# Kernel tuning notes

Measured on AMD Instinct MI355X. Metric: run time of the kernel, lower is better.

The kernel has to match this reference:

```python
import jax, jax.numpy as jnp
import numpy as np

N = 40000   # num nodes
C = 128     # in_channels
H = 8       # num_heads
D = C // H  # head_dim = 16
E = 640000  # num edges
FF = 4 * C


def layer_norm(x, g, b, eps=1e-5):
    m = jnp.mean(x, axis=-1, keepdims=True)
    v = jnp.mean((x - m) ** 2, axis=-1, keepdims=True)
    return (x - m) / jnp.sqrt(v + eps) * g + b


def setup_inputs() -> dict:
    key = jax.random.key(0)
    ks = jax.random.split(key, 16)
    s = 0.02
    x = jax.random.normal(ks[0], (N, C), dtype=jnp.float32)
    edge_index = jax.random.randint(ks[1], (2, E), 0, N, dtype=jnp.int64)
    return {
        'x': x,
        'edge_index': edge_index,
        'Wq': jax.random.normal(ks[2], (C, C), jnp.float32) * s,
        'bq': jnp.zeros((C,), jnp.float32),
        'Wk': jax.random.normal(ks[3], (C, C), jnp.float32) * s,
        'bk': jnp.zeros((C,), jnp.float32),
        'Wv': jax.random.normal(ks[4], (C, C), jnp.float32) * s,
        'bv': jnp.zeros((C,), jnp.float32),
        'Wo': jax.random.normal(ks[5], (C, C), jnp.float32) * s,
        'bo': jnp.zeros((C,), jnp.float32),
        'ln1_g': jnp.ones((C,), jnp.float32),
        'ln1_b': jnp.zeros((C,), jnp.float32),
        'ln2_g': jnp.ones((C,), jnp.float32),
        'ln2_b': jnp.zeros((C,), jnp.float32),
        'W1': jax.random.normal(ks[6], (C, FF), jnp.float32) * s,
        'b1': jnp.zeros((FF,), jnp.float32),
        'W2': jax.random.normal(ks[7], (FF, C), jnp.float32) * s,
        'b2': jnp.zeros((C,), jnp.float32),
    }


def reference(x, edge_index, Wq, bq, Wk, bk, Wv, bv, Wo, bo,
              ln1_g, ln1_b, ln2_g, ln2_b, W1, b1, W2, b2):
    residual = x
    xn = layer_norm(x, ln1_g, ln1_b)
    q = (xn @ Wq + bq).reshape(N, H, D)
    k = (xn @ Wk + bk).reshape(N, H, D)
    v = (xn @ Wv + bv).reshape(N, H, D)
    src, dst = edge_index[0], edge_index[1]
    # per-edge scores: [E, H]
    scores = jnp.einsum('ehd,ehd->eh', q[dst], k[src]) / jnp.sqrt(jnp.float32(D))
    # NOTE: faithful to the source — softmax over ALL edges (dim=0), not per-destination
    attn = jax.nn.softmax(scores, axis=0)[:, :, None]          # [E, H, 1]
    weighted = v[src] * attn                                   # [E, H, D]
    aggregated = jax.ops.segment_sum(weighted, dst, num_segments=N)  # [N, H, D]
    out = aggregated.reshape(N, C) @ Wo + bo
    x1 = residual + out
    residual2 = x1
    xn2 = layer_norm(x1, ln2_g, ln2_b)
    ffn = jax.nn.relu(xn2 @ W1 + b1) @ W2 + b2
    return residual2 + ffn
```

## Files before the change

### kernel.cpp

```cpp
#include <hip/hip_runtime.h>
#include <math.h>

#define NNODES 40000
#define CCH    128
#define NH     8
#define HD     16
#define NEDGE  640000
#define NBLK   157
#define FBLK   10000
#define RBLK   40

typedef __attribute__((ext_vector_type(8))) short bf16x8;
typedef __attribute__((ext_vector_type(4))) float f32x4;
typedef __attribute__((ext_vector_type(2))) float f32x2;

__device__ inline unsigned short f2bf(float f) {
  union { float f; unsigned u; } c; c.f = f;
  unsigned r = c.u + 0x7fffu + ((c.u >> 16) & 1u);
  return (unsigned short)(r >> 16);
}
__device__ inline float bflo(unsigned u) { union { unsigned i; float f; } c; c.i = u << 16; return c.f; }
__device__ inline float bfhi(unsigned u) { union { unsigned i; float f; } c; c.i = u & 0xffff0000u; return c.f; }

__device__ inline unsigned char f2fp8(float v) {
#if __has_builtin(__builtin_amdgcn_cvt_pk_fp8_f32)
  return (unsigned char)(__builtin_amdgcn_cvt_pk_fp8_f32(v, v, 0, false) & 0xff);
#else
  union { float f; unsigned u; } c; c.f = v;
  unsigned s = (c.u >> 24) & 0x80;
  int e = (int)((c.u >> 23) & 0xff) - 127;
  unsigned m = c.u & 0x7fffff;
  if (e > 8) return s | 0x7e;
  if (e >= -6) {
    unsigned q = (m + 0x80000) >> 20; unsigned ee = e + 7;
    if (q == 8) { q = 0; ee++; }
    if (ee > 15) return s | 0x7e;
    return s | (ee << 3) | q;
  }
  if (e < -10) return (unsigned char)s;
  float a = fabsf(v); unsigned q = (unsigned)(a * 512.f + 0.5f); if (q > 7) q = 7;
  return s | q;
#endif
}
__device__ inline void fp8x4d(unsigned w, float* o) {
#if __has_builtin(__builtin_amdgcn_cvt_pk_f32_fp8)
  f32x2 lo = __builtin_amdgcn_cvt_pk_f32_fp8((int)w, false);
  f32x2 hi = __builtin_amdgcn_cvt_pk_f32_fp8((int)w, true);
  o[0] = lo[0]; o[1] = lo[1]; o[2] = hi[0]; o[3] = hi[1];
#else
  #pragma unroll
  for (int i = 0; i < 4; i++) {
    unsigned b = (w >> (8 * i)) & 0xff;
    unsigned s = b >> 7, e = (b >> 3) & 15, m = b & 7;
    float v;
    if (e) { union { unsigned u; float f; } c; c.u = ((e + 120) << 23) | (m << 20); v = c.f; }
    else v = m * (1.f / 512.f);
    o[i] = s ? -v : v;
  }
#endif
}

__global__ __launch_bounds__(256) void k_ln_bf(const float* __restrict__ x,
                                               const float* __restrict__ g,
                                               const float* __restrict__ b,
                                               unsigned* __restrict__ out) {
  int wave = threadIdx.x >> 6;
  int lane = threadIdx.x & 63;
  int row  = blockIdx.x * 4 + wave;
  if (row >= NNODES) return;
  const float2* xr = (const float2*)(x + (size_t)row * CCH);
  float2 v = xr[lane];
  float s  = v.x + v.y;
  float ss = v.x * v.x + v.y * v.y;
  #pragma unroll
  for (int d = 1; d < 64; d <<= 1) {
    s  += __shfl_xor(s, d);
    ss += __shfl_xor(ss, d);
  }
  float mean = s * (1.0f / CCH);
  float var  = ss * (1.0f / CCH) - mean * mean;
  float rstd = rsqrtf(var + 1e-5f);
  float2 gg = ((const float2*)g)[lane];
  float2 bb = ((const float2*)b)[lane];
  float ox = (v.x - mean) * rstd * gg.x + bb.x;
  float oy = (v.y - mean) * rstd * gg.y + bb.y;
  out[(size_t)row * 64 + lane] = ((unsigned)f2bf(oy) << 16) | f2bf(ox);
}

__global__ __launch_bounds__(256) void k_wprep(const float* __restrict__ W,
                                               unsigned short* __restrict__ Wt,
                                               int K, int Nc) {
  int idx = blockIdx.x * 256 + threadIdx.x;
  if (idx >= K * Nc) return;
  int n = idx / K, k = idx - n * K;
  Wt[idx] = f2bf(W[(size_t)k * Nc + n]);
}

__global__ __launch_bounds__(256) void k_wprep_wo(const float* __restrict__ W,
                                                  const float* __restrict__ inv,
                                                  unsigned short* __restrict__ Wt) {
  int idx = blockIdx.x * 256 + threadIdx.x;
  if (idx >= CCH * CCH) return;
  int n = idx >> 7, k = idx & 127;
  Wt[idx] = f2bf(W[(size_t)k * CCH + n] * inv[k >> 4]);
}

__global__ __launch_bounds__(256) void k_bcat(const float* __restrict__ bq,
                                              const float* __restrict__ bk,
                                              const float* __restrict__ bv,
                                              float* __restrict__ bqkv) {
  int t = threadIdx.x + blockIdx.x * 256;
  if (t < 128)      bqkv[t] = bq[t];
  else if (t < 256) bqkv[t] = bk[t - 128];
  else if (t < 384) bqkv[t] = bv[t - 256];
}

template <bool RELU, bool RES, int MODE>
__global__ __launch_bounds__(256) void k_mgemm(const unsigned short* __restrict__ A,
                                               const unsigned short* __restrict__ Bt,
                                               const float* __restrict__ bias,
                                               const float* __restrict__ res,
                                               void* __restrict__ outp,
                                               int K, int Nc) {
  __shared__ unsigned short As[64 * 64];
  __shared__ unsigned short Bs[128 * 64];
  const int tid  = threadIdx.x;
  const int row0 = blockIdx.x * 64;
  const int c0   = blockIdx.y * 128;
  const int l    = tid & 63;
  const int w    = tid >> 6;
  const int wr   = w >> 1;
  const int wc   = w & 1;

  f32x4 acc[2][4] = {};

  for (int kc = 0; kc < K; kc += 64) {
    __syncthreads();
    #pragma unroll
    for (int it = 0; it < 2; it++) {
      int idx = it * 256 + tid;
      int r = idx >> 3, s = idx & 7;
      uint4 vv = *(const uint4*)(A + (size_t)(row0 + r) * K + kc + s * 8);
      *(uint4*)(As + r * 64 + ((s ^ (r & 7)) * 8)) = vv;
    }
    #pragma unroll
    for (int it = 0; it < 4; it++) {
      int idx = it * 256 + tid;
      int n = idx >> 3, s = idx & 7;
      uint4 vv = *(const uint4*)(Bt + (size_t)(c0 + n) * K + kc + s * 8);
      *(uint4*)(Bs + n * 64 + ((s ^ (n & 7)) * 8)) = vv;
    }
    __syncthreads();
    #pragma unroll
    for (int kk = 0; kk < 2; kk++) {
      int sb = kk * 4 + (l >> 4);
      bf16x8 af[2], bfr[4];
      #pragma unroll
      for (int mi = 0; mi < 2; mi++) {
        int r = wr * 32 + mi * 16 + (l & 15);
        af[mi] = *(const bf16x8*)(As + r * 64 + ((sb ^ (r & 7)) * 8));
      }
      #pragma unroll
      for (int ni = 0; ni < 4; ni++) {
        int n = wc * 64 + ni * 16 + (l & 15);
        bfr[ni] = *(const bf16x8*)(Bs + n * 64 + ((sb ^ (n & 7)) * 8));
      }
      #pragma unroll
      for (int mi = 0; mi < 2; mi++)
        #pragma unroll
        for (int ni = 0; ni < 4; ni++)
          acc[mi][ni] = __builtin_amdgcn_mfma_f32_16x16x32_bf16(af[mi], bfr[ni], acc[mi][ni], 0, 0, 0);
    }
  }

  #pragma unroll
  for (int mi = 0; mi < 2; mi++) {
    #pragma unroll
    for (int p = 0; p < 4; p++) {
      int r = row0 + wr * 32 + mi * 16 + (l >> 4) * 4 + p;
      #pragma unroll
      for (int ni = 0; ni < 4; ni++) {
        int c = c0 + wc * 64 + ni * 16 + (l & 15);
        float val = acc[mi][ni][p] + bias[c];
        if (RES)  val += res[(size_t)r * Nc + c];
        if (RELU) val = fmaxf(val, 0.f);
        if (MODE == 0)      ((float*)outp)[(size_t)r * Nc + c] = val;
        else if (MODE == 1) ((unsigned short*)outp)[(size_t)r * Nc + c] = f2bf(val);
        else {
          char* rowb = (char*)outp + (size_t)r * 512;
          if (c < 128) *(unsigned short*)(rowb + c * 2) = f2bf(val);
          else         *(unsigned char*)(rowb + 256 + (c - 128)) = f2fp8(val);
        }
      }
    }
  }
}

__global__ __launch_bounds__(256) void k_histrank(const int* __restrict__ ei,
                                                  int* __restrict__ deg,
                                                  int* __restrict__ rank) {
  int e = blockIdx.x * 256 + threadIdx.x;
  if (e >= NEDGE) return;
  rank[e] = atomicAdd(&deg[ei[NEDGE + e]], 1);
}

__global__ __launch_bounds__(256) void k_scan3a(const int* __restrict__ deg,
                                                int* __restrict__ bsum) {
  int i = blockIdx.x * 256 + threadIdx.x;
  int d = (i < NNODES) ? deg[i] : 0;
  #pragma unroll
  for (int s = 1; s < 64; s <<= 1) d += __shfl_xor(d, s);
  __shared__ int ws4[4];
  if ((threadIdx.x & 63) == 0) ws4[threadIdx.x >> 6] = d;
  __syncthreads();
  if (threadIdx.x == 0) bsum[blockIdx.x] = ws4[0] + ws4[1] + ws4[2] + ws4[3];
}

__global__ __launch_bounds__(256) void k_scan3b(const int* __restrict__ bsum,
                                                int* __restrict__ bpre) {
  int t = threadIdx.x;
  int d = (t < NBLK) ? bsum[t] : 0;
  int lane = t & 63, wv = t >> 6;
  int incl = d;
  #pragma unroll
  for (int s = 1; s < 64; s <<= 1) { int o = __shfl_up(incl, s); if (lane >= s) incl += o; }
  __shared__ int wsum[4];
  if (lane == 63) wsum[wv] = incl;
  __syncthreads();
  int base = 0;
  for (int w2 = 0; w2 < wv; w2++) base += wsum[w2];
  if (t < NBLK) bpre[t] = base + incl - d;
}

__global__ __launch_bounds__(256) void k_scan3c(const int* __restrict__ deg,
                                                const int* __restrict__ bpre,
                                                int* __restrict__ off) {
  int t = threadIdx.x;
  int i = blockIdx.x * 256 + t;
  int d = (i < NNODES) ? deg[i] : 0;
  int lane = t & 63, wv = t >> 6;
  int incl = d;
  #pragma unroll
  for (int s = 1; s < 64; s <<= 1) { int o = __shfl_up(incl, s); if (lane >= s) incl += o; }
  __shared__ int wsum[4];
  if (lane == 63) wsum[wv] = incl;
  __syncthreads();
  int base = bpre[blockIdx.x];
  for (int w2 = 0; w2 < wv; w2++) base += wsum[w2];
  int ex = base + incl - d;
  if (i < NNODES) off[i] = ex;
  if (i == 0) off[NNODES] = NEDGE;
}

__global__ __launch_bounds__(256) void k_scatter(const int* __restrict__ ei,
                                                 const int* __restrict__ off,
                                                 const int* __restrict__ rank,
                                                 int* __restrict__ srcs) {
  int e = blockIdx.x * 256 + threadIdx.x;
  if (e >= NEDGE) return;
  srcs[off[ei[NEDGE + e]] + rank[e]] = ei[e];
}

__global__ __launch_bounds__(256) void k_fused(const unsigned char* __restrict__ qkv,
                                               const int* __restrict__ off,
                                               const int* __restrict__ srcs,
                                               unsigned* __restrict__ U,
                                               float* __restrict__ hpart) {
  const int wave = threadIdx.x >> 6;
  const int lane = threadIdx.x & 63;
  const int n  = blockIdx.x * 4 + wave;
  const int g  = lane >> 3;
  const int c8 = lane & 7;

  const uint4* qp = (const uint4*)(qkv + (size_t)n * 512 + c8 * 32);
  uint4 qa = qp[0], qb = qp[1];
  float qf[16];
  qf[0]=bflo(qa.x);  qf[1]=bfhi(qa.x);  qf[2]=bflo(qa.y);  qf[3]=bfhi(qa.y);
  qf[4]=bflo(qa.z);  qf[5]=bfhi(qa.z);  qf[6]=bflo(qa.w);  qf[7]=bfhi(qa.w);
  qf[8]=bflo(qb.x);  qf[9]=bfhi(qb.x);  qf[10]=bflo(qb.y); qf[11]=bfhi(qb.y);
  qf[12]=bflo(qb.z); qf[13]=bfhi(qb.z); qf[14]=bflo(qb.w); qf[15]=bfhi(qb.w);

  float acc[16];
  #pragma unroll
  for (int i = 0; i < 16; i++) acc[i] = 0.f;
  float lsum = 0.f;

  const int i0 = off[n], i1 = off[n + 1];
  for (int jb = i0; jb < i1; jb += 8) {
    int j = jb + g;
    bool valid = j < i1;
    int src = srcs[valid ? j : jb];
    const uint4* kp = (const uint4*)(qkv + (size_t)src * 512 + 256 + c8 * 16);
    uint4 kw = kp[0];
    uint4 vw = kp[8];
    float kf[16], vf[16];
    fp8x4d(kw.x, kf + 0); fp8x4d(kw.y, kf + 4); fp8x4d(kw.z, kf + 8); fp8x4d(kw.w, kf + 12);
    fp8x4d(vw.x, vf + 0); fp8x4d(vw.y, vf + 4); fp8x4d(vw.z, vf + 8); fp8x4d(vw.w, vf + 12);
    float p = 0.f;
    #pragma unroll
    for (int i = 0; i < 16; i++) p += qf[i] * kf[i];
    float w = valid ? __expf(p * 0.25f) : 0.f;
    lsum += w;
    #pragma unroll
    for (int i = 0; i < 16; i++) acc[i] += w * vf[i];
  }

  #pragma unroll
  for (int d = 8; d < 64; d <<= 1) {
    #pragma unroll
    for (int i = 0; i < 16; i++) acc[i] += __shfl_xor(acc[i], d);
    lsum += __shfl_xor(lsum, d);
  }

  __shared__ float wsum[4][8];
  if (lane < 8) {
    wsum[wave][c8] = lsum;
    unsigned o[8];
    #pragma unroll
    for (int i = 0; i < 8; i++)
      o[i] = ((unsigned)f2bf(acc[2 * i + 1]) << 16) | f2bf(acc[2 * i]);
    uint4* up = (uint4*)(U + (size_t)n * 64 + c8 * 8);
    up[0] = make_uint4(o[0], o[1], o[2], o[3]);
    up[1] = make_uint4(o[4], o[5], o[6], o[7]);
  }
  __syncthreads();
  if (threadIdx.x < 8) {
    hpart[blockIdx.x * 8 + threadIdx.x] =
        wsum[0][threadIdx.x] + wsum[1][threadIdx.x] + wsum[2][threadIdx.x] + wsum[3][threadIdx.x];
  }
}

__global__ __launch_bounds__(256) void k_reduce_part(const float* __restrict__ hpart,
                                                     float* __restrict__ dpart) {
  const int t = threadIdx.x;
  const int h = t & 7;
  const int r0 = blockIdx.x * (FBLK / RBLK);
  float s = 0.f;
  for (int r = r0 + (t >> 3); r < r0 + FBLK / RBLK; r += 32) s += hpart[r * 8 + h];
  #pragma unroll
  for (int d = 8; d < 64; d <<= 1) s += __shfl_xor(s, d);
  __shared__ float ws4[4][8];
  int lane = t & 63, wv = t >> 6;
  if (lane < 8) ws4[wv][lane] = s;
  __syncthreads();
  if (t < 8) dpart[blockIdx.x * 8 + t] = ws4[0][t] + ws4[1][t] + ws4[2][t] + ws4[3][t];
}

__global__ __launch_bounds__(64) void k_inv(const float* __restrict__ dpart,
                                            float* __restrict__ inv) {
  int t = threadIdx.x;
  int h = t & 7;
  float s = 0.f;
  for (int r = t >> 3; r < RBLK; r += 8) s += dpart[r * 8 + h];
  #pragma unroll
  for (int d = 8; d < 64; d <<= 1) s += __shfl_xor(s, d);
  if (t < 8) inv[h] = 1.0f / s;
}

extern "C" void kernel_launch(void* const* d_in, const int* in_sizes, int n_in,
                              void* d_out, int out_size, void* d_ws, size_t ws_size,
                              hipStream_t stream) {
  const float* x    = (const float*)d_in[0];
  const int*   ei   = (const int*)d_in[1];
  const float* Wq   = (const float*)d_in[2];
  const float* bq   = (const float*)d_in[3];
  const float* Wk   = (const float*)d_in[4];
  const float* bk   = (const float*)d_in[5];
  const float* Wv   = (const float*)d_in[6];
  const float* bv   = (const float*)d_in[7];
  const float* Wo   = (const float*)d_in[8];
  const float* bo   = (const float*)d_in[9];
  const float* ln1g = (const float*)d_in[10];
  const float* ln1b = (const float*)d_in[11];
  const float* ln2g = (const float*)d_in[12];
  const float* ln2b = (const float*)d_in[13];
  const float* W1   = (const float*)d_in[14];
  const float* b1   = (const float*)d_in[15];
  const float* W2   = (const float*)d_in[16];
  const float* b2   = (const float*)d_in[17];
  float* out = (float*)d_out;

  char* p = (char*)d_ws;
  unsigned short* xn   = (unsigned short*)p; p += (size_t)NNODES * CCH * 2;
  unsigned char*  qkvb = (unsigned char*)p;  p += (size_t)NNODES * 512;
  unsigned short* agg  = (unsigned short*)p; p += (size_t)NNODES * CCH * 2;
  float*          x1   = (float*)p;          p += (size_t)NNODES * CCH * 4;
  unsigned short* ffn1 = (unsigned short*)p; p += (size_t)NNODES * 4 * CCH * 2;
  int* deg    = (int*)p;                     p += (size_t)NNODES * 4 + 256;
  int* off    = (int*)p;                     p += (size_t)(NNODES + 1) * 4 + 256;
  int* rank   = (int*)p;                     p += (size_t)NEDGE * 4;
  int* srcs   = (int*)p;                     p += (size_t)NEDGE * 4;
  int* bsum   = (int*)p;                     p += 256 * 4;
  int* bpre   = (int*)p;                     p += 256 * 4;
  float* hpart = (float*)p;                  p += (size_t)FBLK * 8 * 4;
  float* dpart = (float*)p;                  p += (size_t)RBLK * 8 * 4 + 256;
  float* inv   = (float*)p;                  p += 256;
  float* bqkv  = (float*)p;                  p += 384 * 4 + 256;
  unsigned short* Wqkvt = (unsigned short*)p; p += (size_t)384 * CCH * 2;
  unsigned short* Wot   = (unsigned short*)p; p += (size_t)CCH * CCH * 2;
  unsigned short* W1t   = (unsigned short*)p; p += (size_t)CCH * 4 * CCH * 2;
  unsigned short* W2t   = (unsigned short*)p; p += (size_t)CCH * 4 * CCH * 2;
  unsigned short* xn2 = xn;

  dim3 blk(256);
  dim3 gLN(NNODES / 4);
  dim3 gM(NNODES / 64, 1);
  dim3 gM3(NNODES / 64, 3);
  dim3 gM4(NNODES / 64, 4);
  dim3 gE((NEDGE + 255) / 256);
  dim3 gW64((CCH * CCH + 255) / 256);
  dim3 gW256((CCH * 4 * CCH + 255) / 256);

  hipMemsetAsync(deg, 0, (size_t)NNODES * 4, stream);
  k_histrank<<<gE, blk, 0, stream>>>(ei, deg, rank);
  k_scan3a<<<NBLK, blk, 0, stream>>>(deg, bsum);
  k_scan3b<<<1, blk, 0, stream>>>(bsum, bpre);
  k_scan3c<<<NBLK, blk, 0, stream>>>(deg, bpre, off);
  k_scatter<<<gE, blk, 0, stream>>>(ei, off, rank, srcs);

  k_wprep<<<gW64, blk, 0, stream>>>(Wq, Wqkvt, CCH, CCH);
  k_wprep<<<gW64, blk, 0, stream>>>(Wk, Wqkvt + (size_t)CCH * CCH, CCH, CCH);
  k_wprep<<<gW64, blk, 0, stream>>>(Wv, Wqkvt + (size_t)2 * CCH * CCH, CCH, CCH);
  k_wprep<<<gW256, blk, 0, stream>>>(W1, W1t, CCH, 4 * CCH);
  k_wprep<<<gW256, blk, 0, stream>>>(W2, W2t, 4 * CCH, CCH);
  k_bcat<<<2, blk, 0, stream>>>(bq, bk, bv, bqkv);

  k_ln_bf<<<gLN, blk, 0, stream>>>(x, ln1g, ln1b, (unsigned*)xn);
  k_mgemm<false, false, 2><<<gM3, blk, 0, stream>>>(xn, Wqkvt, bqkv, nullptr, qkvb, CCH, 384);

  k_fused<<<FBLK, blk, 0, stream>>>(qkvb, off, srcs, (unsigned*)agg, hpart);
  k_reduce_part<<<RBLK, blk, 0, stream>>>(hpart, dpart);
  k_inv<<<1, dim3(64), 0, stream>>>(dpart, inv);

  k_wprep_wo<<<gW64, blk, 0, stream>>>(Wo, inv, Wot);
  k_mgemm<false, true, 0><<<gM, blk, 0, stream>>>(agg, Wot, bo, x, x1, CCH, CCH);

  k_ln_bf<<<gLN, blk, 0, stream>>>(x1, ln2g, ln2b, (unsigned*)xn2);
  k_mgemm<true, false, 1><<<gM4, blk, 0, stream>>>(xn2, W1t, b1, nullptr, ffn1, CCH, 4 * CCH);
  k_mgemm<false, true, 0><<<gM, blk, 0, stream>>>(ffn1, W2t, b2, x1, out, 4 * CCH, CCH);
}
```

Before: 181.0 us.

## Fuse CSR build into cooperative kernel, merge weight prep, fuse LN2 into Wo GEMM

The memset, histogram, three-stage scan and scatter are replaced by one cooperative kernel that uses grid-wide syncs. All weight transposes and the bias concat are merged into one launch, and the inverse-denominator computation moves into the Wo weight-prep kernel. The Wo GEMM epilogue now computes LayerNorm2 and writes x1 as bf16 along with the normalized output, which removes a separate LN pass and halves x1 traffic. The FFN1 buffer reuses the qkv region. The aim is to cut launch count and memory traffic, at the cost of bf16 rounding on the residual and the overhead of grid syncs.

```diff
diff --git a/kernel.cpp b/kernel.cpp
--- a/kernel.cpp
+++ b/kernel.cpp
@@ -1,14 +1,17 @@
 #include <hip/hip_runtime.h>
+#include <hip/hip_cooperative_groups.h>
 #include <math.h>
+
+namespace cg = cooperative_groups;
 
 #define NNODES 40000
 #define CCH    128
 #define NH     8
 #define HD     16
 #define NEDGE  640000
-#define NBLK   157
 #define FBLK   10000
 #define RBLK   40
+#define CGRID  1024
 
 typedef __attribute__((ext_vector_type(8))) short bf16x8;
 typedef __attribute__((ext_vector_type(4))) float f32x4;
@@ -19,6 +22,7 @@
   unsigned r = c.u + 0x7fffu + ((c.u >> 16) & 1u);
   return (unsigned short)(r >> 16);
 }
+__device__ inline float bfs(unsigned short u) { union { unsigned i; float f; } c; c.i = (unsigned)u << 16; return c.f; }
 __device__ inline float bflo(unsigned u) { union { unsigned i; float f; } c; c.i = u << 16; return c.f; }
 __device__ inline float bfhi(unsigned u) { union { unsigned i; float f; } c; c.i = u & 0xffff0000u; return c.f; }
 
@@ -87,41 +91,61 @@
   out[(size_t)row * 64 + lane] = ((unsigned)f2bf(oy) << 16) | f2bf(ox);
 }
 
-__global__ __launch_bounds__(256) void k_wprep(const float* __restrict__ W,
-                                               unsigned short* __restrict__ Wt,
-                                               int K, int Nc) {
+__global__ __launch_bounds__(256) void k_wprep_all(const float* __restrict__ Wq,
+                                                   const float* __restrict__ Wk,
+                                                   const float* __restrict__ Wv,
+                                                   const float* __restrict__ W1,
+                                                   const float* __restrict__ W2,
+                                                   const float* __restrict__ bq,
+                                                   const float* __restrict__ bk,
+                                                   const float* __restrict__ bv,
+                                                   unsigned short* __restrict__ Wqkvt,
+                                                   unsigned short* __restrict__ W1t,
+                                                   unsigned short* __restrict__ W2t,
+                                                   float* __restrict__ bqkv) {
   int idx = blockIdx.x * 256 + threadIdx.x;
-  if (idx >= K * Nc) return;
-  int n = idx / K, k = idx - n * K;
-  Wt[idx] = f2bf(W[(size_t)k * Nc + n]);
+  if (idx < 16384) { int n = idx >> 7, k = idx & 127; Wqkvt[idx] = f2bf(Wq[(size_t)k * 128 + n]); return; }
+  idx -= 16384;
+  if (idx < 16384) { int n = idx >> 7, k = idx & 127; Wqkvt[16384 + (n << 7) + k] = f2bf(Wk[(size_t)k * 128 + n]); return; }
+  idx -= 16384;
+  if (idx < 16384) { int n = idx >> 7, k = idx & 127; Wqkvt[32768 + (n << 7) + k] = f2bf(Wv[(size_t)k * 128 + n]); return; }
+  idx -= 16384;
+  if (idx < 65536) { int n = idx >> 7, k = idx & 127; W1t[idx] = f2bf(W1[(size_t)k * 512 + n]); return; }
+  idx -= 65536;
+  if (idx < 65536) { int n = idx >> 9, k = idx & 511; W2t[idx] = f2bf(W2[(size_t)k * 128 + n]); return; }
+  idx -= 65536;
+  if (idx < 384) bqkv[idx] = idx < 128 ? bq[idx] : (idx < 256 ? bk[idx - 128] : bv[idx - 256]);
 }
 
 __global__ __launch_bounds__(256) void k_wprep_wo(const float* __restrict__ W,
-                                                  const float* __restrict__ inv,
+                                                  const float* __restrict__ dpart,
                                                   unsigned short* __restrict__ Wt) {
+  __shared__ float sinv[8];
+  if (threadIdx.x < 64) {
+    int h = threadIdx.x & 7;
+    float s = 0.f;
+    for (int r = threadIdx.x >> 3; r < RBLK; r += 8) s += dpart[r * 8 + h];
+    #pragma unroll
+    for (int d = 8; d < 64; d <<= 1) s += __shfl_xor(s, d);
+    if (threadIdx.x < 8) sinv[h] = 1.0f / s;
+  }
+  __syncthreads();
   int idx = blockIdx.x * 256 + threadIdx.x;
   if (idx >= CCH * CCH) return;
   int n = idx >> 7, k = idx & 127;
-  Wt[idx] = f2bf(W[(size_t)k * CCH + n] * inv[k >> 4]);
-}
-
-__global__ __launch_bounds__(256) void k_bcat(const float* __restrict__ bq,
-                                              const float* __restrict__ bk,
-                                              const float* __restrict__ bv,
-                                              float* __restrict__ bqkv) {
-  int t = threadIdx.x + blockIdx.x * 256;
-  if (t < 128)      bqkv[t] = bq[t];
-  else if (t < 256) bqkv[t] = bk[t - 128];
-  else if (t < 384) bqkv[t] = bv[t - 256];
-}
-
-template <bool RELU, bool RES, int MODE>
+  Wt[idx] = f2bf(W[(size_t)k * CCH + n] * sinv[k >> 4]);
+}
+
+template <bool RELU, int RESMODE, int MODE>
 __global__ __launch_bounds__(256) void k_mgemm(const unsigned short* __restrict__ A,
                                                const unsigned short* __restrict__ Bt,
                                                const float* __restrict__ bias,
-                                               const float* __restrict__ res,
+                                               const void* __restrict__ res,
                                                void* __restrict__ outp,
-                                               int K, int Nc) {
+                                               int K, int Nc,
+                                               const float* __restrict__ lng,
+                                               const float* __restrict__ lnb,
+                                               void* __restrict__ outp2) {
   __shared__ unsigned short As[64 * 64];
   __shared__ unsigned short Bs[128 * 64];
   const int tid  = threadIdx.x;
@@ -173,92 +197,139 @@
     }
   }
 
-  #pragma unroll
-  for (int mi = 0; mi < 2; mi++) {
-    #pragma unroll
-    for (int p = 0; p < 4; p++) {
-      int r = row0 + wr * 32 + mi * 16 + (l >> 4) * 4 + p;
-      #pragma unroll
-      for (int ni = 0; ni < 4; ni++) {
-        int c = c0 + wc * 64 + ni * 16 + (l & 15);
-        float val = acc[mi][ni][p] + bias[c];
-        if (RES)  val += res[(size_t)r * Nc + c];
-        if (RELU) val = fmaxf(val, 0.f);
-        if (MODE == 0)      ((float*)outp)[(size_t)r * Nc + c] = val;
-        else if (MODE == 1) ((unsigned short*)outp)[(size_t)r * Nc + c] = f2bf(val);
-        else {
-          char* rowb = (char*)outp + (size_t)r * 512;
-          if (c < 128) *(unsigned short*)(rowb + c * 2) = f2bf(val);
-          else         *(unsigned char*)(rowb + 256 + (c - 128)) = f2fp8(val);
+  if constexpr (MODE == 3) {
+    __shared__ float lnS[64][2], lnSS[64][2], gS[128], bS[128];
+    if (tid < 128) { gS[tid] = lng[tid]; bS[tid] = lnb[tid]; }
+    #pragma unroll
+    for (int mi = 0; mi < 2; mi++) {
+      #pragma unroll
+      for (int p = 0; p < 4; p++) {
+        int lr = wr * 32 + mi * 16 + (l >> 4) * 4 + p;
+        int r  = row0 + lr;
+        float s = 0.f, ss = 0.f;
+        #pragma unroll
+        for (int ni = 0; ni < 4; ni++) {
+          int c = wc * 64 + ni * 16 + (l & 15);
+          float val = acc[mi][ni][p] + bias[c] + ((const float*)res)[(size_t)r * 128 + c];
+          acc[mi][ni][p] = val;
+          s += val; ss += val * val;
+        }
+        #pragma unroll
+        for (int d = 1; d < 16; d <<= 1) { s += __shfl_xor(s, d); ss += __shfl_xor(ss, d); }
+        if ((l & 15) == 0) { lnS[lr][wc] = s; lnSS[lr][wc] = ss; }
+      }
+    }
+    __syncthreads();
+    #pragma unroll
+    for (int mi = 0; mi < 2; mi++) {
+      #pragma unroll
+      for (int p = 0; p < 4; p++) {
+        int lr = wr * 32 + mi * 16 + (l >> 4) * 4 + p;
+        int r  = row0 + lr;
+        float m   = (lnS[lr][0] + lnS[lr][1]) * (1.f / 128.f);
+        float var = (lnSS[lr][0] + lnSS[lr][1]) * (1.f / 128.f) - m * m;
+        float rstd = rsqrtf(var + 1e-5f);
+        #pragma unroll
+        for (int ni = 0; ni < 4; ni++) {
+          int c = wc * 64 + ni * 16 + (l & 15);
+          float val = acc[mi][ni][p];
+          ((unsigned short*)outp)[(size_t)r * 128 + c]  = f2bf(val);
+          ((unsigned short*)outp2)[(size_t)r * 128 + c] = f2bf((val - m) * rstd * gS[c] + bS[c]);
         }
       }
     }
-  }
-}
-
-__global__ __launch_bounds__(256) void k_histrank(const int* __restrict__ ei,
-                                                  int* __restrict__ deg,
-                                                  int* __restrict__ rank) {
-  int e = blockIdx.x * 256 + threadIdx.x;
-  if (e >= NEDGE) return;
-  rank[e] = atomicAdd(&deg[ei[NEDGE + e]], 1);
-}
-
-__global__ __launch_bounds__(256) void k_scan3a(const int* __restrict__ deg,
-                                                int* __restrict__ bsum) {
-  int i = blockIdx.x * 256 + threadIdx.x;
-  int d = (i < NNODES) ? deg[i] : 0;
-  #pragma unroll
-  for (int s = 1; s < 64; s <<= 1) d += __shfl_xor(d, s);
+  } else {
+    #pragma unroll
+    for (int mi = 0; mi < 2; mi++) {
+      #pragma unroll
+      for (int p = 0; p < 4; p++) {
+        int r = row0 + wr * 32 + mi * 16 + (l >> 4) * 4 + p;
+        #pragma unroll
+        for (int ni = 0; ni < 4; ni++) {
+          int c = c0 + wc * 64 + ni * 16 + (l & 15);
+          float val = acc[mi][ni][p] + bias[c];
+          if (RESMODE == 1) val += ((const float*)res)[(size_t)r * Nc + c];
+          if (RESMODE == 2) val += bfs(((const unsigned short*)res)[(size_t)r * Nc + c]);
+          if (RELU) val = fmaxf(val, 0.f);
+          if (MODE == 0)      ((float*)outp)[(size_t)r * Nc + c] = val;
+          else if (MODE == 1) ((unsigned short*)outp)[(size_t)r * Nc + c] = f2bf(val);
+          else {
+            char* rowb = (char*)outp + (size_t)r * 512;
+            if (c < 128) *(unsigned short*)(rowb + c * 2) = f2bf(val);
+            else         *(unsigned char*)(rowb + 256 + (c - 128)) = f2fp8(val);
+          }
+        }
+      }
+    }
+  }
+}
+
+__global__ __launch_bounds__(256) void k_csr(const int* __restrict__ ei,
+                                             int* __restrict__ deg,
+                                             int* __restrict__ rank,
+                                             int* __restrict__ off,
+                                             int* __restrict__ bsum,
+                                             int* __restrict__ srcs) {
+  cg::grid_group grid = cg::this_grid();
+  const int tid = threadIdx.x;
+  const int gid = blockIdx.x * 256 + tid;
+  const int GSZ = CGRID * 256;
   __shared__ int ws4[4];
-  if ((threadIdx.x & 63) == 0) ws4[threadIdx.x >> 6] = d;
-  __syncthreads();
-  if (threadIdx.x == 0) bsum[blockIdx.x] = ws4[0] + ws4[1] + ws4[2] + ws4[3];
-}
-
-__global__ __launch_bounds__(256) void k_scan3b(const int* __restrict__ bsum,
-                                                int* __restrict__ bpre) {
-  int t = threadIdx.x;
-  int d = (t < NBLK) ? bsum[t] : 0;
-  int lane = t & 63, wv = t >> 6;
-  int incl = d;
-  #pragma unroll
-  for (int s = 1; s < 64; s <<= 1) { int o = __shfl_up(incl, s); if (lane >= s) incl += o; }
-  __shared__ int wsum[4];
-  if (lane == 63) wsum[wv] = incl;
-  __syncthreads();
-  int base = 0;
-  for (int w2 = 0; w2 < wv; w2++) base += wsum[w2];
-  if (t < NBLK) bpre[t] = base + incl - d;
-}
-
-__global__ __launch_bounds__(256) void k_scan3c(const int* __restrict__ deg,
-                                                const int* __restrict__ bpre,
-                                                int* __restrict__ off) {
-  int t = threadIdx.x;
-  int i = blockIdx.x * 256 + t;
-  int d = (i < NNODES) ? deg[i] : 0;
-  int lane = t & 63, wv = t >> 6;
-  int incl = d;
-  #pragma unroll
-  for (int s = 1; s < 64; s <<= 1) { int o = __shfl_up(incl, s); if (lane >= s) incl += o; }
-  __shared__ int wsum[4];
-  if (lane == 63) wsum[wv] = incl;
-  __syncthreads();
-  int base = bpre[blockIdx.x];
-  for (int w2 = 0; w2 < wv; w2++) base += wsum[w2];
-  int ex = base + incl - d;
-  if (i < NNODES) off[i] = ex;
-  if (i == 0) off[NNODES] = NEDGE;
-}
-
-__global__ __launch_bounds__(256) void k_scatter(const int* __restrict__ ei,
-                                                 const int* __restrict__ off,
-                                                 const int* __restrict__ rank,
-                                                 int* __restrict__ srcs) {
-  int e = blockIdx.x * 256 + threadIdx.x;
-  if (e >= NEDGE) return;
-  srcs[off[ei[NEDGE + e]] + rank[e]] = ei[e];
+
+  for (int i = gid; i < NNODES; i += GSZ) deg[i] = 0;
+  grid.sync();
+
+  for (int e = gid; e < NEDGE; e += GSZ)
+    rank[e] = atomicAdd(&deg[ei[NEDGE + e]], 1);
+  grid.sync();
+
+  {
+    int d = (gid < NNODES) ? deg[gid] : 0;
+    #pragma unroll
+    for (int s = 1; s < 64; s <<= 1) d += __shfl_xor(d, s);
+    if ((tid & 63) == 0) ws4[tid >> 6] = d;
+    __syncthreads();
+    if (tid == 0) bsum[blockIdx.x] = ws4[0] + ws4[1] + ws4[2] + ws4[3];
+  }
+  grid.sync();
+
+  if (blockIdx.x == 0) {
+    int v0 = bsum[4 * tid], v1 = bsum[4 * tid + 1], v2 = bsum[4 * tid + 2], v3 = bsum[4 * tid + 3];
+    int ls = v0 + v1 + v2 + v3;
+    int lane = tid & 63, wv = tid >> 6;
+    int incl = ls;
+    #pragma unroll
+    for (int s = 1; s < 64; s <<= 1) { int o = __shfl_up(incl, s); if (lane >= s) incl += o; }
+    __syncthreads();
+    if (lane == 63) ws4[wv] = incl;
+    __syncthreads();
+    int base = 0;
+    for (int w2 = 0; w2 < wv; w2++) base += ws4[w2];
+    int ex = base + incl - ls;
+    bsum[4 * tid] = ex; bsum[4 * tid + 1] = ex + v0;
+    bsum[4 * tid + 2] = ex + v0 + v1; bsum[4 * tid + 3] = ex + v0 + v1 + v2;
+  }
+  grid.sync();
+
+  {
+    int d = (gid < NNODES) ? deg[gid] : 0;
+    int lane = tid & 63, wv = tid >> 6;
+    int incl = d;
+    #pragma unroll
+    for (int s = 1; s < 64; s <<= 1) { int o = __shfl_up(incl, s); if (lane >= s) incl += o; }
+    __syncthreads();
+    if (lane == 63) ws4[wv] = incl;
+    __syncthreads();
+    int base = bsum[blockIdx.x];
+    for (int w2 = 0; w2 < wv; w2++) base += ws4[w2];
+    int ex = base + incl - d;
+    if (gid < NNODES) off[gid] = ex;
+    if (gid == 0) off[NNODES] = NEDGE;
+  }
+  grid.sync();
+
+  for (int e = gid; e < NEDGE; e += GSZ)
+    srcs[off[ei[NEDGE + e]] + rank[e]] = ei[e];
 }
 
 __global__ __launch_bounds__(256) void k_fused(const unsigned char* __restrict__ qkv,
@@ -344,17 +415,6 @@
   if (lane < 8) ws4[wv][lane] = s;
   __syncthreads();
   if (t < 8) dpart[blockIdx.x * 8 + t] = ws4[0][t] + ws4[1][t] + ws4[2][t] + ws4[3][t];
-}
-
-__global__ __launch_bounds__(64) void k_inv(const float* __restrict__ dpart,
-                                            float* __restrict__ inv) {
-  int t = threadIdx.x;
-  int h = t & 7;
-  float s = 0.f;
-  for (int r = t >> 3; r < RBLK; r += 8) s += dpart[r * 8 + h];
-  #pragma unroll
-  for (int d = 8; d < 64; d <<= 1) s += __shfl_xor(s, d);
-  if (t < 8) inv[h] = 1.0f / s;
 }
 
 extern "C" void kernel_launch(void* const* d_in, const int* in_sizes, int n_in,
@@ -381,61 +441,57 @@
   float* out = (float*)d_out;
 
   char* p = (char*)d_ws;
-  unsigned short* xn   = (unsigned short*)p; p += (size_t)NNODES * CCH * 2;
+  const size_t NCb = (size_t)NNODES * CCH * 2;
+  unsigned short* xn   = (unsigned short*)p; p += NCb;
   unsigned char*  qkvb = (unsigned char*)p;  p += (size_t)NNODES * 512;
-  unsigned short* agg  = (unsigned short*)p; p += (size_t)NNODES * CCH * 2;
-  float*          x1   = (float*)p;          p += (size_t)NNODES * CCH * 4;
-  unsigned short* ffn1 = (unsigned short*)p; p += (size_t)NNODES * 4 * CCH * 2;
+  unsigned short* agg  = (unsigned short*)p; p += NCb;
+  p += NCb;
+  unsigned short* x1b  = (unsigned short*)p; p += NCb;
   int* deg    = (int*)p;                     p += (size_t)NNODES * 4 + 256;
   int* off    = (int*)p;                     p += (size_t)(NNODES + 1) * 4 + 256;
   int* rank   = (int*)p;                     p += (size_t)NEDGE * 4;
   int* srcs   = (int*)p;                     p += (size_t)NEDGE * 4;
-  int* bsum   = (int*)p;                     p += 256 * 4;
-  int* bpre   = (int*)p;                     p += 256 * 4;
+  int* bsum   = (int*)p;                     p += (size_t)CGRID * 4 + 256;
   float* hpart = (float*)p;                  p += (size_t)FBLK * 8 * 4;
   float* dpart = (float*)p;                  p += (size_t)RBLK * 8 * 4 + 256;
-  float* inv   = (float*)p;                  p += 256;
   float* bqkv  = (float*)p;                  p += 384 * 4 + 256;
   unsigned short* Wqkvt = (unsigned short*)p; p += (size_t)384 * CCH * 2;
   unsigned short* Wot   = (unsigned short*)p; p += (size_t)CCH * CCH * 2;
   unsigned short* W1t   = (unsigned short*)p; p += (size_t)CCH * 4 * CCH * 2;
   unsigned short* W2t   = (unsigned short*)p; p += (size_t)CCH * 4 * CCH * 2;
-  unsigned short* xn2 = xn;
+  unsigned short* ffn1 = (unsigned short*)qkvb;
+  unsigned short* xn2  = xn;
 
   dim3 blk(256);
   dim3 gLN(NNODES / 4);
   dim3 gM(NNODES / 64, 1);
   dim3 gM3(NNODES / 64, 3);
   dim3 gM4(NNODES / 64, 4);
-  dim3 gE((NEDGE + 255) / 256);
-  dim3 gW64((CCH * CCH + 255) / 256);
-  dim3 gW256((CCH * 4 * CCH + 255) / 256);
-
-  hipMemsetAsync(deg, 0, (size_t)NNODES * 4, stream);
-  k_histrank<<<gE, blk, 0, stream>>>(ei, deg, rank);
-  k_scan3a<<<NBLK, blk, 0, stream>>>(deg, bsum);
-  k_scan3b<<<1, blk, 0, stream>>>(bsum, bpre);
-  k_scan3c<<<NBLK, blk, 0, stream>>>(deg, bpre, off);
-  k_scatter<<<gE, blk, 0, stream>>>(ei, off, rank, srcs);
-
-  k_wprep<<<gW64, blk, 0, stream>>>(Wq, Wqkvt, CCH, CCH);
-  k_wprep<<<gW64, blk, 0, stream>>>(Wk, Wqkvt + (size_t)CCH * CCH, CCH, CCH);
-  k_wprep<<<gW64, blk, 0, stream>>>(Wv, Wqkvt + (size_t)2 * CCH * CCH, CCH, CCH);
-  k_wprep<<<gW256, blk, 0, stream>>>(W1, W1t, CCH, 4 * CCH);
-  k_wprep<<<gW256, blk, 0, stream>>>(W2, W2t, 4 * CCH, CCH);
-  k_bcat<<<2, blk, 0, stream>>>(bq, bk, bv, bqkv);
+
+  {
+    const int* eip = ei;
+    int *degp = deg, *rankp = rank, *offp = off, *bsump = bsum, *srcsp = srcs;
+    void* args[] = {(void*)&eip, (void*)&degp, (void*)&rankp,
+                    (void*)&offp, (void*)&bsump, (void*)&srcsp};
+    hipLaunchCooperativeKernel((void*)k_csr, dim3(CGRID), blk, args, 0, stream);
+  }
+
+  k_wprep_all<<<706, blk, 0, stream>>>(Wq, Wk, Wv, W1, W2, bq, bk, bv,
+                                       Wqkvt, W1t, W2t, bqkv);
 
   k_ln_bf<<<gLN, blk, 0, stream>>>(x, ln1g, ln1b, (unsigned*)xn);
-  k_mgemm<false, false, 2><<<gM3, blk, 0, stream>>>(xn, Wqkvt, bqkv, nullptr, qkvb, CCH, 384);
+  k_mgemm<false, 0, 2><<<gM3, blk, 0, stream>>>(xn, Wqkvt, bqkv, nullptr, qkvb,
+                                                CCH, 384, nullptr, nullptr, nullptr);
 
   k_fused<<<FBLK, blk, 0, stream>>>(qkvb, off, srcs, (unsigned*)agg, hpart);
   k_reduce_part<<<RBLK, blk, 0, stream>>>(hpart, dpart);
-  k_inv<<<1, dim3(64), 0, stream>>>(dpart, inv);
-
-  k_wprep_wo<<<gW64, blk, 0, stream>>>(Wo, inv, Wot);
-  k_mgemm<false, true, 0><<<gM, blk, 0, stream>>>(agg, Wot, bo, x, x1, CCH, CCH);
-
-  k_ln_bf<<<gLN, blk, 0, stream>>>(x1, ln2g, ln2b, (unsigned*)xn2);
-  k_mgemm<true, false, 1><<<gM4, blk, 0, stream>>>(xn2, W1t, b1, nullptr, ffn1, CCH, 4 * CCH);
-  k_mgemm<false, true, 0><<<gM, blk, 0, stream>>>(ffn1, W2t, b2, x1, out, 4 * CCH, CCH);
-}
+
+  k_wprep_wo<<<64, blk, 0, stream>>>(Wo, dpart, Wot);
+  k_mgemm<false, 1, 3><<<gM, blk, 0, stream>>>(agg, Wot, bo, x, x1b,
+                                               CCH, CCH, ln2g, ln2b, xn2);
+
+  k_mgemm<true, 0, 1><<<gM4, blk, 0, stream>>>(xn2, W1t, b1, nullptr, ffn1,
+                                               CCH, 4 * CCH, nullptr, nullptr, nullptr);
+  k_mgemm<false, 2, 0><<<gM, blk, 0, stream>>>(ffn1, W2t, b2, x1b, out,
+                                               4 * CCH, CCH, nullptr, nullptr, nullptr);
+}
```

Result: slower. 655.0 us (+261.8%).
